# Performance work log

Hardware: AMD Instinct MI355X
Metric: run time of the kernel (lower is better)

Reference implementation:

```python
import jax, jax.numpy as jnp
import numpy as np

B, C, D = 16384, 2048, 256
THR = 0.8       # threshold
M_NEG = 0.3     # margin_neg (margin_pos is unused in the original forward)
EPS = 1e-8      # torch.nn.CosineSimilarity norm clamp


def setup_inputs() -> dict:
    key = jax.random.key(0)
    k1, k2 = jax.random.split(key)
    preds = jax.random.normal(k1, (B, D), dtype=jnp.float32)
    cls = jax.random.randint(k2, (B,), 0, C)
    labels = jax.nn.one_hot(cls, C, dtype=jnp.float32)  # [B, C] one-hot soft labels
    return {"preds": preds, "labels": labels}


def reference(preds, labels):
    # --- append(): running-mean centroids over rows with labels >= THR ---
    # The sequential EMA with counter c -> c/(c+1)*old + 1/(c+1)*new is exactly the
    # arithmetic mean of the contributing preds, so compute it as a masked mean.
    mask = labels >= THR                                  # [B, C]
    cnt = mask.sum(axis=0)                                # [C]
    exists = cnt > 0                                      # which centroids exist in the dict
    maskf = mask.astype(preds.dtype)
    centroids = (maskf.T @ preds) / jnp.maximum(cnt, 1).astype(preds.dtype)[:, None]  # [C, D]

    pn = preds / jnp.maximum(jnp.linalg.norm(preds, axis=1, keepdims=True), EPS)  # [B, D]

    # --- dist_positive: 1 - cos(pred, sum_{label>0} label[c] * centroid[c]) ---
    cmb = jnp.where(labels > 0, labels, 0.0) @ centroids  # [B, D]
    cmbn = cmb / jnp.maximum(jnp.linalg.norm(cmb, axis=1, keepdims=True), EPS)
    pos = 1.0 - jnp.sum(pn * cmbn, axis=1)                # [B]

    # --- dist_negative: mean over existing centroids with label < 1-THR of
    #     relu(margin_neg - (1 - cos(pred, centroid))) ---
    cn = centroids / jnp.maximum(jnp.linalg.norm(centroids, axis=1, keepdims=True), EPS)
    cos_all = pn @ cn.T                                   # [B, C]
    neg_mask = (labels < 1.0 - THR) & exists[None, :]     # [B, C]
    hinge = jnp.maximum(M_NEG - (1.0 - cos_all), 0.0)
    adds = jnp.maximum(neg_mask.sum(axis=1), 1).astype(preds.dtype)  # [B]
    neg = (hinge * neg_mask).sum(axis=1) / adds           # [B]

    return jnp.mean(pos) + jnp.mean(neg)
```

## Files before the change

### kernel.cpp

```cpp
#include <hip/hip_runtime.h>
#include <hip/hip_bf16.h>

constexpr int BB = 16384;
constexpr int CC = 2048;
constexpr int DD = 256;
constexpr float THR   = 0.8f;
constexpr float EPSN  = 1e-8f;

typedef __bf16 bf16x8 __attribute__((ext_vector_type(8)));
typedef float  f32x4  __attribute__((ext_vector_type(4)));

constexpr int ROWSLOTS = 64;

__global__ __launch_bounds__(256) void k_prep(const float* __restrict__ labels,
                                              const float* __restrict__ preds,
                                              int* __restrict__ cls,
                                              int* __restrict__ cnt,
                                              int* __restrict__ rowlist,
                                              unsigned short* __restrict__ pn,
                                              float* __restrict__ out) {
  if (blockIdx.x < 2048) {
    if (blockIdx.x == 0 && threadIdx.x == 0) *out = 0.f;
    constexpr size_t total = (size_t)BB * CC / 4;
    size_t q = (size_t)blockIdx.x * 256 + threadIdx.x;
    const float4* l4 = reinterpret_cast<const float4*>(labels);
    for (; q < total; q += 2048 * 256) {
      float4 v = l4[q];
      if (v.x >= THR || v.y >= THR || v.z >= THR || v.w >= THR) {
        int f = (int)(q * 4);
        int row = f >> 11;
        int col = f & (CC - 1);
        int c = col + (v.x >= THR ? 0 : v.y >= THR ? 1 : v.z >= THR ? 2 : 3);
        cls[row] = c;
        int s = atomicAdd(&cnt[c], 1);
        if (s < ROWSLOTS) rowlist[c * ROWSLOTS + s] = row;
      }
    }
  } else {
    int b = (blockIdx.x - 2048) * 4 + (threadIdx.x >> 6);
    int lane = threadIdx.x & 63;
    float4 v = reinterpret_cast<const float4*>(preds + (size_t)b * DD)[lane];
    float s = v.x * v.x + v.y * v.y + v.z * v.z + v.w * v.w;
#pragma unroll
    for (int o = 32; o > 0; o >>= 1) s += __shfl_xor(s, o);
    float inv = 1.0f / fmaxf(sqrtf(s), EPSN);
    union { ushort4 u4; unsigned short us[4]; } o;
    float f0 = v.x * inv, f1 = v.y * inv, f2 = v.z * inv, f3 = v.w * inv;
    __bf16 h0 = (__bf16)f0, h1 = (__bf16)f1, h2 = (__bf16)f2, h3 = (__bf16)f3;
    o.us[0] = *reinterpret_cast<unsigned short*>(&h0);
    o.us[1] = *reinterpret_cast<unsigned short*>(&h1);
    o.us[2] = *reinterpret_cast<unsigned short*>(&h2);
    o.us[3] = *reinterpret_cast<unsigned short*>(&h3);
    reinterpret_cast<ushort4*>(pn + (size_t)b * DD)[lane] = o.u4;
  }
}

__global__ __launch_bounds__(256) void k_cn(
    const float* __restrict__ preds, const int* __restrict__ cnt,
    const int* __restrict__ rowlist, unsigned short* __restrict__ cn,
    int* __restrict__ exists, int* __restrict__ Ecnt) {
  int c = blockIdx.x;
  int t = threadIdx.x;
  int n = cnt[c];
  int nn = n < ROWSLOTS ? n : ROWSLOTS;
  float sum = 0.f;
  for (int i = 0; i < nn; ++i) {
    int row = rowlist[c * ROWSLOTS + i];
    sum += preds[(size_t)row * DD + t];
  }
  float mean = sum / (float)(n > 0 ? n : 1);
  float s = mean * mean;
#pragma unroll
  for (int o = 32; o > 0; o >>= 1) s += __shfl_xor(s, o);
  __shared__ float red[4];
  int wave = t >> 6, lane = t & 63;
  if (lane == 0) red[wave] = s;
  __syncthreads();
  float tot = red[0] + red[1] + red[2] + red[3];
  float inv = 1.0f / fmaxf(sqrtf(tot), EPSN);
  __bf16 h = (__bf16)(mean * inv);
  cn[c * DD + t] = *reinterpret_cast<unsigned short*>(&h);
  if (t == 0) {
    exists[c] = (n > 0) ? 1 : 0;
    if (n > 0) atomicAdd(Ecnt, 1);
  }
}


__device__ __forceinline__ void stage32k(char* lds, const char* gsrc_row0,
                                         int tid, int ksbyte) {
#pragma unroll
  for (int i = 0; i < 4; ++i) {
    int L = i * 8192 + tid * 16;
    int row = L >> 7;
    int kb  = (L & 127) ^ ((row & 7) << 4);
    const char* g = gsrc_row0 + (size_t)row * (DD * 2) + ksbyte + kb;
    __builtin_amdgcn_global_load_lds(
        (const __attribute__((address_space(1))) unsigned int*)g,
        (__attribute__((address_space(3))) unsigned int*)(lds + L), 16, 0, 0);
  }
}

__device__ __forceinline__ bf16x8 ldfrag(const char* buf, int row, int kb) {
  return *reinterpret_cast<const bf16x8*>(buf + row * 128 + (kb ^ ((row & 7) << 4)));
}

__global__ __launch_bounds__(512, 2) void k_loss(
    const unsigned short* __restrict__ pn, const unsigned short* __restrict__ cn,
    const int* __restrict__ cls, const int* __restrict__ exists,
    const int* __restrict__ Ecnt, float* __restrict__ out) {
  constexpr int BM = 256, BN = 256;
  __shared__ __align__(16) char sA[2][BM * 64 * 2];
  __shared__ __align__(16) char sB[2][BN * 64 * 2];
  __shared__ float red[8];

  int bid = blockIdx.x;
  int nb = (bid & 7) * 64 + (bid >> 3);
  int mtile = nb & 63;
  int ntile = nb >> 6;
  int rowbase = mtile * BM, colbase = ntile * BN;
  int tid = threadIdx.x, w = tid >> 6, lane = tid & 63;
  int wm = w >> 2, wn = w & 3;
  int r16 = lane & 15, khi = lane >> 4;
  int arow0 = wm * 128 + r16;
  int brow0 = wn * 64 + r16;

  const char* pnB = (const char*)pn + (size_t)rowbase * (DD * 2);
  const char* cnB = (const char*)cn + (size_t)colbase * (DD * 2);

  f32x4 acc[8][4];
#pragma unroll
  for (int m = 0; m < 8; ++m)
#pragma unroll
    for (int n = 0; n < 4; ++n) acc[m][n] = {0.f, 0.f, 0.f, 0.f};

  stage32k(sA[0], pnB, tid, 0);
  stage32k(sB[0], cnB, tid, 0);
  __syncthreads();

  int cur = 0;
#pragma unroll
  for (int ks = 0; ks < 4; ++ks) {
    if (ks < 3) {
      stage32k(sA[cur ^ 1], pnB, tid, (ks + 1) * 128);
      stage32k(sB[cur ^ 1], cnB, tid, (ks + 1) * 128);
    }
    const char* bufA = sA[cur];
    const char* bufB = sB[cur];
#pragma unroll
    for (int kk = 0; kk < 2; ++kk) {
      int kb = kk * 64 + khi * 16;
      bf16x8 b[4];
#pragma unroll
      for (int n = 0; n < 4; ++n) b[n] = ldfrag(bufB, brow0 + n * 16, kb);
#pragma unroll
      for (int m = 0; m < 8; ++m) {
        bf16x8 a = ldfrag(bufA, arow0 + m * 16, kb);
#pragma unroll
        for (int n = 0; n < 4; ++n)
          acc[m][n] = __builtin_amdgcn_mfma_f32_16x16x32_bf16(a, b[n], acc[m][n], 0, 0, 0);
      }
    }
    __syncthreads();
    cur ^= 1;
  }

  int E = *Ecnt;
  float inv_B = 1.0f / (float)BB;
  float inv_neg = inv_B / (float)((E - 1) > 0 ? (E - 1) : 1);
  int grow0 = rowbase + wm * 128;

  int clsr[8][4];
#pragma unroll
  for (int m = 0; m < 8; ++m)
#pragma unroll
    for (int r = 0; r < 4; ++r) clsr[m][r] = cls[grow0 + m * 16 + khi * 4 + r];
  int exs[4];
#pragma unroll
  for (int n = 0; n < 4; ++n) exs[n] = exists[colbase + wn * 64 + n * 16 + r16];

  float local = 0.f;
#pragma unroll
  for (int m = 0; m < 8; ++m)
#pragma unroll
    for (int n = 0; n < 4; ++n) {
      int ccol = colbase + wn * 64 + n * 16 + r16;
#pragma unroll
      for (int r = 0; r < 4; ++r) {
        float v = acc[m][n][r];
        if (ccol == clsr[m][r])
          local += (1.0f - v) * inv_B;
        else if (exs[n])
          local += fmaxf(v - 0.7f, 0.f) * inv_neg;
      }
    }

#pragma unroll
  for (int o = 32; o > 0; o >>= 1) local += __shfl_xor(local, o);
  if (lane == 0) red[w] = local;
  __syncthreads();
  if (tid == 0) {
    float t = 0.f;
#pragma unroll
    for (int i = 0; i < 8; ++i) t += red[i];
    atomicAdd(out, t);
  }
}

extern "C" void kernel_launch(void* const* d_in, const int* in_sizes, int n_in,
                              void* d_out, int out_size, void* d_ws, size_t ws_size,
                              hipStream_t stream) {
  const float* preds  = (const float*)d_in[0];
  const float* labels = (const float*)d_in[1];
  float* out = (float*)d_out;

  char* ws = (char*)d_ws;
  int*            cnt     = (int*)(ws + 0);
  int*            Ecnt    = (int*)(ws + 8192);
  int*            cls     = (int*)(ws + 8256);
  int*            rowlist = (int*)(ws + 73792);
  int*            exists  = (int*)(ws + 598080);
  unsigned short* pn      = (unsigned short*)(ws + 606272);
  unsigned short* cn      = (unsigned short*)(ws + 8994880);

  hipMemsetAsync(ws, 0, 8256, stream);
  k_prep<<<6144, 256, 0, stream>>>(labels, preds, cls, cnt, rowlist, pn, out);
  k_cn<<<CC, 256, 0, stream>>>(preds, cnt, rowlist, cn, exists, Ecnt);
  k_loss<<<512, 512, 0, stream>>>(pn, cn, cls, exists, Ecnt, out);
}
```

Before: 96.25 us.

## Fuse centroid build into GEMM-loss kernel via cooperative grid sync

Removes the memset, the global atomic counters and the separate centroid kernel. Each of 256 cooperative blocks scans cls to build row lists for its 8 classes in shared memory, computes their normalized centroids, then does a grid-wide sync before the bf16 MFMA loss GEMM. Each block now processes two M tiles, and the count of existing centroids is recomputed per block from the exists array. This saves launches and global atomics, at the cost of a grid barrier, a redundant 16K-element cls scan in every block, and only 256 resident blocks instead of 512.

Result: slower. 135.2 us (+40.5%).

```diff
diff --git a/kernel.cpp b/kernel.cpp
--- a/kernel.cpp
+++ b/kernel.cpp
@@ -1,5 +1,8 @@
 #include <hip/hip_runtime.h>
 #include <hip/hip_bf16.h>
+#include <hip/hip_cooperative_groups.h>
+
+namespace cg = cooperative_groups;
 
 constexpr int BB = 16384;
 constexpr int CC = 2048;
@@ -10,15 +13,13 @@
 typedef __bf16 bf16x8 __attribute__((ext_vector_type(8)));
 typedef float  f32x4  __attribute__((ext_vector_type(4)));
 
-constexpr int ROWSLOTS = 64;
-
-__global__ __launch_bounds__(256) void k_prep(const float* __restrict__ labels,
-                                              const float* __restrict__ preds,
-                                              int* __restrict__ cls,
-                                              int* __restrict__ cnt,
-                                              int* __restrict__ rowlist,
-                                              unsigned short* __restrict__ pn,
-                                              float* __restrict__ out) {
+constexpr int SLOTS = 48;
+
+__global__ __launch_bounds__(256) void k_scan_pn(const float* __restrict__ labels,
+                                                 const float* __restrict__ preds,
+                                                 int* __restrict__ cls,
+                                                 unsigned short* __restrict__ pn,
+                                                 float* __restrict__ out) {
   if (blockIdx.x < 2048) {
     if (blockIdx.x == 0 && threadIdx.x == 0) *out = 0.f;
     constexpr size_t total = (size_t)BB * CC / 4;
@@ -30,10 +31,7 @@
         int f = (int)(q * 4);
         int row = f >> 11;
         int col = f & (CC - 1);
-        int c = col + (v.x >= THR ? 0 : v.y >= THR ? 1 : v.z >= THR ? 2 : 3);
-        cls[row] = c;
-        int s = atomicAdd(&cnt[c], 1);
-        if (s < ROWSLOTS) rowlist[c * ROWSLOTS + s] = row;
+        cls[row] = col + (v.x >= THR ? 0 : v.y >= THR ? 1 : v.z >= THR ? 2 : 3);
       }
     }
   } else {
@@ -55,37 +53,6 @@
   }
 }
 
-__global__ __launch_bounds__(256) void k_cn(
-    const float* __restrict__ preds, const int* __restrict__ cnt,
-    const int* __restrict__ rowlist, unsigned short* __restrict__ cn,
-    int* __restrict__ exists, int* __restrict__ Ecnt) {
-  int c = blockIdx.x;
-  int t = threadIdx.x;
-  int n = cnt[c];
-  int nn = n < ROWSLOTS ? n : ROWSLOTS;
-  float sum = 0.f;
-  for (int i = 0; i < nn; ++i) {
-    int row = rowlist[c * ROWSLOTS + i];
-    sum += preds[(size_t)row * DD + t];
-  }
-  float mean = sum / (float)(n > 0 ? n : 1);
-  float s = mean * mean;
-#pragma unroll
-  for (int o = 32; o > 0; o >>= 1) s += __shfl_xor(s, o);
-  __shared__ float red[4];
-  int wave = t >> 6, lane = t & 63;
-  if (lane == 0) red[wave] = s;
-  __syncthreads();
-  float tot = red[0] + red[1] + red[2] + red[3];
-  float inv = 1.0f / fmaxf(sqrtf(tot), EPSN);
-  __bf16 h = (__bf16)(mean * inv);
-  cn[c * DD + t] = *reinterpret_cast<unsigned short*>(&h);
-  if (t == 0) {
-    exists[c] = (n > 0) ? 1 : 0;
-    if (n > 0) atomicAdd(Ecnt, 1);
-  }
-}
-
 
 __device__ __forceinline__ void stage32k(char* lds, const char* gsrc_row0,
                                          int tid, int ksbyte) {
@@ -105,105 +72,159 @@
   return *reinterpret_cast<const bf16x8*>(buf + row * 128 + (kb ^ ((row & 7) << 4)));
 }
 
-__global__ __launch_bounds__(512, 2) void k_loss(
-    const unsigned short* __restrict__ pn, const unsigned short* __restrict__ cn,
-    const int* __restrict__ cls, const int* __restrict__ exists,
-    const int* __restrict__ Ecnt, float* __restrict__ out) {
+__global__ __launch_bounds__(512, 2) void k_main(
+    const float* __restrict__ preds, const unsigned short* __restrict__ pn,
+    const int* __restrict__ cls, unsigned short* __restrict__ cn,
+    int* __restrict__ exists, float* __restrict__ out) {
   constexpr int BM = 256, BN = 256;
   __shared__ __align__(16) char sA[2][BM * 64 * 2];
   __shared__ __align__(16) char sB[2][BN * 64 * 2];
+  __shared__ int   s_cnt[8];
+  __shared__ int   s_rows[8][SLOTS];
+  __shared__ float s_red[2][4];
   __shared__ float red[8];
 
   int bid = blockIdx.x;
-  int nb = (bid & 7) * 64 + (bid >> 3);
-  int mtile = nb & 63;
-  int ntile = nb >> 6;
-  int rowbase = mtile * BM, colbase = ntile * BN;
-  int tid = threadIdx.x, w = tid >> 6, lane = tid & 63;
+  int tid = threadIdx.x;
+
+  if (tid < 8) s_cnt[tid] = 0;
+  __syncthreads();
+  int c0 = bid * 8;
+  for (int i = tid; i < BB; i += 512) {
+    int c = cls[i];
+    if ((c >> 3) == bid) {
+      int slot = atomicAdd(&s_cnt[c & 7], 1);
+      if (slot < SLOTS) s_rows[c & 7][slot] = i;
+    }
+  }
+  __syncthreads();
+  {
+    int sub = tid >> 8, dim = tid & 255;
+    for (int g = 0; g < 4; ++g) {
+      int lc = g * 2 + sub;
+      int c = c0 + lc;
+      int n = s_cnt[lc];
+      int nn = n < SLOTS ? n : SLOTS;
+      float sum = 0.f;
+      for (int i = 0; i < nn; ++i)
+        sum += preds[(size_t)s_rows[lc][i] * DD + dim];
+      float mean = sum / (float)(n > 0 ? n : 1);
+      float ss = mean * mean;
+#pragma unroll
+      for (int o = 32; o > 0; o >>= 1) ss += __shfl_xor(ss, o);
+      int wv = (tid >> 6) & 3;
+      if ((tid & 63) == 0) s_red[sub][wv] = ss;
+      __syncthreads();
+      float tot = s_red[sub][0] + s_red[sub][1] + s_red[sub][2] + s_red[sub][3];
+      float inv = 1.0f / fmaxf(sqrtf(tot), EPSN);
+      __bf16 h = (__bf16)(mean * inv);
+      cn[(size_t)c * DD + dim] = *reinterpret_cast<unsigned short*>(&h);
+      if (dim == 0) exists[c] = (n > 0) ? 1 : 0;
+      __syncthreads();
+    }
+  }
+
+  cg::this_grid().sync();
+
+  int w = tid >> 6, lane = tid & 63;
+  float ee = 0.f;
+  for (int i = tid; i < CC; i += 512) ee += (float)exists[i];
+#pragma unroll
+  for (int o = 32; o > 0; o >>= 1) ee += __shfl_xor(ee, o);
+  if (lane == 0) red[w] = ee;
+  __syncthreads();
+  int E = (int)(red[0] + red[1] + red[2] + red[3] +
+                red[4] + red[5] + red[6] + red[7]);
+  float inv_B = 1.0f / (float)BB;
+  float inv_neg = inv_B / (float)((E - 1) > 0 ? (E - 1) : 1);
+  __syncthreads();
+
   int wm = w >> 2, wn = w & 3;
   int r16 = lane & 15, khi = lane >> 4;
   int arow0 = wm * 128 + r16;
   int brow0 = wn * 64 + r16;
-
-  const char* pnB = (const char*)pn + (size_t)rowbase * (DD * 2);
+  int ntile = bid & 7;
+  int colbase = ntile * BN;
   const char* cnB = (const char*)cn + (size_t)colbase * (DD * 2);
 
-  f32x4 acc[8][4];
-#pragma unroll
-  for (int m = 0; m < 8; ++m)
-#pragma unroll
-    for (int n = 0; n < 4; ++n) acc[m][n] = {0.f, 0.f, 0.f, 0.f};
-
-  stage32k(sA[0], pnB, tid, 0);
-  stage32k(sB[0], cnB, tid, 0);
-  __syncthreads();
-
-  int cur = 0;
-#pragma unroll
-  for (int ks = 0; ks < 4; ++ks) {
-    if (ks < 3) {
-      stage32k(sA[cur ^ 1], pnB, tid, (ks + 1) * 128);
-      stage32k(sB[cur ^ 1], cnB, tid, (ks + 1) * 128);
-    }
-    const char* bufA = sA[cur];
-    const char* bufB = sB[cur];
-#pragma unroll
-    for (int kk = 0; kk < 2; ++kk) {
-      int kb = kk * 64 + khi * 16;
-      bf16x8 b[4];
-#pragma unroll
-      for (int n = 0; n < 4; ++n) b[n] = ldfrag(bufB, brow0 + n * 16, kb);
-#pragma unroll
-      for (int m = 0; m < 8; ++m) {
-        bf16x8 a = ldfrag(bufA, arow0 + m * 16, kb);
-#pragma unroll
-        for (int n = 0; n < 4; ++n)
-          acc[m][n] = __builtin_amdgcn_mfma_f32_16x16x32_bf16(a, b[n], acc[m][n], 0, 0, 0);
-      }
-    }
+  for (int tt = 0; tt < 2; ++tt) {
+    int mtile = (bid >> 3) * 2 + tt;
+    int rowbase = mtile * BM;
+    const char* pnB = (const char*)pn + (size_t)rowbase * (DD * 2);
+
+    f32x4 acc[8][4];
+#pragma unroll
+    for (int m = 0; m < 8; ++m)
+#pragma unroll
+      for (int n = 0; n < 4; ++n) acc[m][n] = {0.f, 0.f, 0.f, 0.f};
+
+    stage32k(sA[0], pnB, tid, 0);
+    stage32k(sB[0], cnB, tid, 0);
     __syncthreads();
-    cur ^= 1;
-  }
-
-  int E = *Ecnt;
-  float inv_B = 1.0f / (float)BB;
-  float inv_neg = inv_B / (float)((E - 1) > 0 ? (E - 1) : 1);
-  int grow0 = rowbase + wm * 128;
-
-  int clsr[8][4];
-#pragma unroll
-  for (int m = 0; m < 8; ++m)
-#pragma unroll
-    for (int r = 0; r < 4; ++r) clsr[m][r] = cls[grow0 + m * 16 + khi * 4 + r];
-  int exs[4];
-#pragma unroll
-  for (int n = 0; n < 4; ++n) exs[n] = exists[colbase + wn * 64 + n * 16 + r16];
-
-  float local = 0.f;
-#pragma unroll
-  for (int m = 0; m < 8; ++m)
-#pragma unroll
-    for (int n = 0; n < 4; ++n) {
-      int ccol = colbase + wn * 64 + n * 16 + r16;
-#pragma unroll
-      for (int r = 0; r < 4; ++r) {
-        float v = acc[m][n][r];
-        if (ccol == clsr[m][r])
-          local += (1.0f - v) * inv_B;
-        else if (exs[n])
-          local += fmaxf(v - 0.7f, 0.f) * inv_neg;
-      }
-    }
-
-#pragma unroll
-  for (int o = 32; o > 0; o >>= 1) local += __shfl_xor(local, o);
-  if (lane == 0) red[w] = local;
-  __syncthreads();
-  if (tid == 0) {
-    float t = 0.f;
-#pragma unroll
-    for (int i = 0; i < 8; ++i) t += red[i];
-    atomicAdd(out, t);
+
+    int cur = 0;
+#pragma unroll
+    for (int ks = 0; ks < 4; ++ks) {
+      if (ks < 3) {
+        stage32k(sA[cur ^ 1], pnB, tid, (ks + 1) * 128);
+        stage32k(sB[cur ^ 1], cnB, tid, (ks + 1) * 128);
+      }
+      const char* bufA = sA[cur];
+      const char* bufB = sB[cur];
+#pragma unroll
+      for (int kk = 0; kk < 2; ++kk) {
+        int kb = kk * 64 + khi * 16;
+        bf16x8 b[4];
+#pragma unroll
+        for (int n = 0; n < 4; ++n) b[n] = ldfrag(bufB, brow0 + n * 16, kb);
+#pragma unroll
+        for (int m = 0; m < 8; ++m) {
+          bf16x8 a = ldfrag(bufA, arow0 + m * 16, kb);
+#pragma unroll
+          for (int n = 0; n < 4; ++n)
+            acc[m][n] = __builtin_amdgcn_mfma_f32_16x16x32_bf16(a, b[n], acc[m][n], 0, 0, 0);
+        }
+      }
+      __syncthreads();
+      cur ^= 1;
+    }
+
+    int grow0 = rowbase + wm * 128;
+    int clsr[8][4];
+#pragma unroll
+    for (int m = 0; m < 8; ++m)
+#pragma unroll
+      for (int r = 0; r < 4; ++r) clsr[m][r] = cls[grow0 + m * 16 + khi * 4 + r];
+    int exs[4];
+#pragma unroll
+    for (int n = 0; n < 4; ++n) exs[n] = exists[colbase + wn * 64 + n * 16 + r16];
+
+    float local = 0.f;
+#pragma unroll
+    for (int m = 0; m < 8; ++m)
+#pragma unroll
+      for (int n = 0; n < 4; ++n) {
+        int ccol = colbase + wn * 64 + n * 16 + r16;
+#pragma unroll
+        for (int r = 0; r < 4; ++r) {
+          float v = acc[m][n][r];
+          if (ccol == clsr[m][r])
+            local += (1.0f - v) * inv_B;
+          else if (exs[n])
+            local += fmaxf(v - 0.7f, 0.f) * inv_neg;
+        }
+      }
+
+#pragma unroll
+    for (int o = 32; o > 0; o >>= 1) local += __shfl_xor(local, o);
+    if (lane == 0) red[w] = local;
+    __syncthreads();
+    if (tid == 0) {
+      float t = 0.f;
+#pragma unroll
+      for (int i = 0; i < 8; ++i) t += red[i];
+      atomicAdd(out, t);
+    }
   }
 }
 
@@ -215,16 +236,20 @@
   float* out = (float*)d_out;
 
   char* ws = (char*)d_ws;
-  int*            cnt     = (int*)(ws + 0);
-  int*            Ecnt    = (int*)(ws + 8192);
-  int*            cls     = (int*)(ws + 8256);
-  int*            rowlist = (int*)(ws + 73792);
-  int*            exists  = (int*)(ws + 598080);
-  unsigned short* pn      = (unsigned short*)(ws + 606272);
-  unsigned short* cn      = (unsigned short*)(ws + 8994880);
-
-  hipMemsetAsync(ws, 0, 8256, stream);
-  k_prep<<<6144, 256, 0, stream>>>(labels, preds, cls, cnt, rowlist, pn, out);
-  k_cn<<<CC, 256, 0, stream>>>(preds, cnt, rowlist, cn, exists, Ecnt);
-  k_loss<<<512, 512, 0, stream>>>(pn, cn, cls, exists, Ecnt, out);
-}
+  int*            cls    = (int*)(ws + 0);
+  int*            exists = (int*)(ws + 65536);
+  unsigned short* pn     = (unsigned short*)(ws + 73728);
+  unsigned short* cn     = (unsigned short*)(ws + 8462336);
+
+  k_scan_pn<<<6144, 256, 0, stream>>>(labels, preds, cls, pn, out);
+
+  const float* preds_a = preds;
+  const unsigned short* pn_a = pn;
+  const int* cls_a = cls;
+  unsigned short* cn_a = cn;
+  int* exists_a = exists;
+  float* out_a = out;
+  void* args[] = {&preds_a, &pn_a, &cls_a, &cn_a, &exists_a, &out_a};
+  hipLaunchCooperativeKernel(reinterpret_cast<void*>(k_main),
+                             dim3(256), dim3(512), args, 0, stream);
+}
```
